# Kernel tuning notes

Measured on AMD Instinct MI355X. Metric: run time of the kernel, lower is better.

## Reference

```python
import jax, jax.numpy as jnp
import numpy as np

B, N, NT = 64, 1024, 100
DIM, KD, NH, D = 256, 16, 8, 64
DH = D * NH            # 512
NH_KD = KD * NH        # 128
H_KV = DH + NH_KD      # 640
PROJ_IN = DH + 1000    # 1512
NUM_OFFSETS = 10000    # 100x100 grid of (|dx|,|dy|)
EPS = 1e-5


def _bn_params(key, n):
    k1, k2, k3, k4 = jax.random.split(key, 4)
    gamma = 1.0 + 0.1 * jax.random.normal(k1, (n,), jnp.float32)
    beta = 0.1 * jax.random.normal(k2, (n,), jnp.float32)
    mean = 0.1 * jax.random.normal(k3, (n,), jnp.float32)
    var = 0.5 + jax.random.uniform(k4, (n,), jnp.float32)
    return gamma, beta, mean, var


def setup_inputs() -> dict:
    key = jax.random.key(0)
    ks = jax.random.split(key, 9)
    x = jax.random.normal(ks[0], (B, N, DIM), jnp.float32)
    text = jax.random.normal(ks[1], (NT, DIM), jnp.float32)
    kv_w = jax.random.normal(ks[2], (H_KV, DIM), jnp.float32) * (DIM ** -0.5)
    q_w = jax.random.normal(ks[3], (NH_KD, DIM), jnp.float32) * (DIM ** -0.5)
    proj_w = jax.random.normal(ks[4], (DIM, PROJ_IN), jnp.float32) * (PROJ_IN ** -0.5)
    kv_g, kv_b, kv_m, kv_v = _bn_params(ks[5], H_KV)
    q_g, q_b, q_m, q_v = _bn_params(ks[6], NH_KD)
    proj_g, proj_b, proj_m, proj_v = _bn_params(ks[7], DIM)
    biases = 0.02 * jax.random.normal(ks[8], (NH, NUM_OFFSETS), jnp.float32)
    return {
        'x': x, 'text': text,
        'kv_w': kv_w, 'kv_g': kv_g, 'kv_b': kv_b, 'kv_m': kv_m, 'kv_v': kv_v,
        'q_w': q_w, 'q_g': q_g, 'q_b': q_b, 'q_m': q_m, 'q_v': q_v,
        'proj_w': proj_w, 'proj_g': proj_g, 'proj_b': proj_b, 'proj_m': proj_m, 'proj_v': proj_v,
        'biases': biases, 'H': 32, 'W': 32,
    }


def _linear_bn(x, w, g, b, m, v):
    # Linear (no bias) followed by BatchNorm1d in eval mode, per feature.
    y = x @ w.T
    return (y - m) * (g * jax.lax.rsqrt(v + EPS)) + b


def _hardswish(x):
    return x * jnp.clip(x + 3.0, 0.0, 6.0) * (1.0 / 6.0)


def _bias_idx(nt, h, w):
    # text tokens laid on (row, col) grid of width 100; image tokens on HxW grid.
    t = jnp.arange(nt)
    p1x, p1y = t // 100, t % 100
    n = jnp.arange(h * w)
    p2x, p2y = n // w, n % w
    # offset id = |dx| * 100 + |dy| (first-appearance order of the offset dict)
    return jnp.abs(p1x[:, None] - p2x[None, :]) * 100 + jnp.abs(p1y[:, None] - p2y[None, :])


def reference(x, text, kv_w, kv_g, kv_b, kv_m, kv_v,
              q_w, q_g, q_b, q_m, q_v,
              proj_w, proj_g, proj_b, proj_m, proj_v,
              biases, H, W):
    b, n, _ = x.shape
    nt = text.shape[0]
    scale = KD ** -0.5

    kv = _linear_bn(x, kv_w, kv_g, kv_b, kv_m, kv_v).reshape(b, n, NH, KD + D)
    k = kv[..., :KD]                 # [B, N, NH, KD]
    v = kv[..., KD:]                 # [B, N, NH, D]
    q = _linear_bn(text, q_w, q_g, q_b, q_m, q_v).reshape(nt, NH, KD)  # [NT, NH, KD]

    idx = _bias_idx(nt, H, W)        # [NT, N] int32
    attn = jnp.einsum('thd,bnhd->bhtn', q, k) * scale + biases[:, idx]  # [B, NH, NT, N]
    attn = jax.nn.softmax(attn, axis=-1)

    v_flat = v.reshape(b, n, DH)                                    # [B, N, DH]
    attn_feat = attn.reshape(b, NH * nt, n).transpose(0, 2, 1)      # [B, N, NH*NT]
    comp = jnp.zeros((b, n, 1000 - nt * NH), x.dtype)
    v_cat = jnp.concatenate([v_flat, attn_feat, comp], axis=-1)     # [B, N, DH+1000]

    return _linear_bn(_hardswish(v_cat), proj_w, proj_g, proj_b, proj_m, proj_v)
```

## Files before the change

### kernel.cpp

```cpp
#include <hip/hip_runtime.h>
#include <hip/hip_bf16.h>

#define B_    64
#define N_    1024
#define NT_   100
#define DIM_  256
#define KD_   16
#define NH_   8
#define D_    64
#define DH_   512
#define HKV_  640
#define PROJIN_ 1512
#define KCAT_ 1312
#define EPS_  1e-5f
#define M_    (B_*N_)

typedef __attribute__((ext_vector_type(8))) short bf16x8;
typedef __attribute__((ext_vector_type(4))) float f32x4;

__device__ __forceinline__ int iabs(int x){ return x<0?-x:x; }
__device__ __forceinline__ unsigned short bfr(float f){ __hip_bfloat16 h=__float2bfloat16(f); return *(unsigned short*)&h; }
__device__ __forceinline__ float bfl(unsigned short u){ union{unsigned int i;float f;}c; c.i=(unsigned int)u<<16; return c.f; }

#define GLDS16(src, dst) __builtin_amdgcn_global_load_lds( \
    (const __attribute__((address_space(1))) void*)(src),  \
    (__attribute__((address_space(3))) void*)(dst), 16, 0, 0)

__global__ __launch_bounds__(256) void p0_cvt(
    const float* __restrict__ kvw, const float* __restrict__ pw,
    unsigned short* __restrict__ kvwb, unsigned short* __restrict__ pwb)
{
    const size_t stride = (size_t)gridDim.x * 256;
    const size_t i0 = (size_t)blockIdx.x * 256 + threadIdx.x;
    for (size_t q = i0; q < (size_t)HKV_*DIM_/4; q += stride) {
        float4 v = ((const float4*)kvw)[q];
        ushort4 o; o.x=bfr(v.x); o.y=bfr(v.y); o.z=bfr(v.z); o.w=bfr(v.w);
        ((ushort4*)kvwb)[q] = o;
    }
    for (size_t q = i0; q < (size_t)DIM_*KCAT_/4; q += stride) {
        const int row = (int)(q / (KCAT_/4)), cq = (int)(q % (KCAT_/4));
        float4 v = ((const float4*)(pw + (size_t)row*PROJIN_))[cq];
        ushort4 o; o.x=bfr(v.x); o.y=bfr(v.y); o.z=bfr(v.z); o.w=bfr(v.w);
        ((ushort4*)pwb)[q] = o;
    }
}

__global__ __launch_bounds__(256,2) void k1g(
    const float* __restrict__ x, const unsigned short* __restrict__ wb,
    const float* __restrict__ g, const float* __restrict__ bb,
    const float* __restrict__ mn, const float* __restrict__ vr,
    unsigned short* __restrict__ kb, unsigned short* __restrict__ vb)
{
    __shared__ unsigned short As[128*32];
    __shared__ unsigned short Bs[128*32];
    __shared__ unsigned short Ls[64*128];
    const int tid = threadIdx.x;
    const int wave = tid >> 6, lane = tid & 63;
    const int logical = (blockIdx.x & 7) * 320 + (blockIdx.x >> 3);
    const int nblk = logical % 5, mblk = logical / 5;
    const int m0 = mblk * 128, n0 = nblk * 128;
    const int wm = (wave >> 1) * 64, wn = (wave & 1) * 64;
    const int srow = lane >> 2, scol = (lane & 3) * 8;
    const int sr = tid >> 1, sh = (tid & 1) * 16;
    f32x4 acc[4][4];
    #pragma unroll
    for (int i=0;i<4;i++)
        #pragma unroll
        for (int j=0;j<4;j++) acc[i][j] = (f32x4){0.f,0.f,0.f,0.f};

    for (int k0 = 0; k0 < DIM_; k0 += 32) {
        #pragma unroll
        for (int i = 0; i < 2; i++) {
            const int rr = (wave*2 + i)*16 + srow;
            GLDS16(wb + (size_t)(n0+rr)*DIM_ + k0 + scol, Bs + (wave*2+i)*512);
        }
        {
            const float* xs = x + (size_t)(m0+sr)*DIM_ + k0 + sh;
            float4 v0 = ((const float4*)xs)[0], v1 = ((const float4*)xs)[1];
            float4 v2 = ((const float4*)xs)[2], v3 = ((const float4*)xs)[3];
            ushort4 a0, a1, b0, b1;
            a0.x=bfr(v0.x); a0.y=bfr(v0.y); a0.z=bfr(v0.z); a0.w=bfr(v0.w);
            a1.x=bfr(v1.x); a1.y=bfr(v1.y); a1.z=bfr(v1.z); a1.w=bfr(v1.w);
            b0.x=bfr(v2.x); b0.y=bfr(v2.y); b0.z=bfr(v2.z); b0.w=bfr(v2.w);
            b1.x=bfr(v3.x); b1.y=bfr(v3.y); b1.z=bfr(v3.z); b1.w=bfr(v3.w);
            *(ushort4*)&As[sr*32 + sh]      = a0;
            *(ushort4*)&As[sr*32 + sh + 4]  = a1;
            *(ushort4*)&As[sr*32 + sh + 8]  = b0;
            *(ushort4*)&As[sr*32 + sh + 12] = b1;
        }
        __syncthreads();
        bf16x8 af[4], bfv[4];
        #pragma unroll
        for (int f = 0; f < 4; f++) {
            af[f]  = *(const bf16x8*)&As[(wm + f*16 + (lane&15))*32 + (lane>>4)*8];
            bfv[f] = *(const bf16x8*)&Bs[(wn + f*16 + (lane&15))*32 + (lane>>4)*8];
        }
        #pragma unroll
        for (int fi = 0; fi < 4; fi++)
            #pragma unroll
            for (int fj = 0; fj < 4; fj++)
                acc[fi][fj] = __builtin_amdgcn_mfma_f32_16x16x32_bf16(af[fi], bfv[fj], acc[fi][fj], 0,0,0);
        __syncthreads();
    }

    #pragma unroll
    for (int pass = 0; pass < 2; ++pass) {
        if ((wave >> 1) == pass) {
            #pragma unroll
            for (int fj = 0; fj < 4; fj++) {
                const int col = wn + fj*16 + (lane & 15);
                const int gcol = n0 + col;
                const float s = g[gcol] * rsqrtf(vr[gcol] + EPS_);
                const float o = bb[gcol] - mn[gcol] * s;
                const bool vcol = (gcol - (gcol/80)*80) >= 16;
                #pragma unroll
                for (int fi = 0; fi < 4; fi++)
                    #pragma unroll
                    for (int r = 0; r < 4; r++) {
                        float v = acc[fi][fj][r] * s + o;
                        if (vcol) v = v * fminf(fmaxf(v + 3.f, 0.f), 6.f) * (1.f/6.f);
                        Ls[(fi*16 + (lane>>4)*4 + r)*128 + col] = bfr(v);
                    }
            }
        }
        __syncthreads();
        #pragma unroll
        for (int it = 0; it < 4; ++it) {
            const int row = it*16 + (tid >> 4);
            const int c8  = tid & 15;
            bf16x8 val = *(const bf16x8*)&Ls[row*128 + c8*8];
            const int gcol = n0 + c8*8;
            const int h = gcol / 80, rem = gcol - h*80;
            const int m = m0 + pass*64 + row;
            unsigned short* dst = (rem < 16)
                ? (kb + (size_t)m*128 + h*16 + rem)
                : (vb + (size_t)m*512 + h*64 + (rem - 16));
            *(bf16x8*)dst = val;
        }
        __syncthreads();
    }
}

__global__ __launch_bounds__(128) void k2_q(
    const float* __restrict__ text, const float* __restrict__ q_w,
    const float* __restrict__ g, const float* __restrict__ bb,
    const float* __restrict__ mn, const float* __restrict__ vr,
    float* __restrict__ q_out)
{
    __shared__ float ts[DIM_];
    const int t = blockIdx.x, j = threadIdx.x;
    for (int i = threadIdx.x; i < DIM_; i += 128) ts[i] = text[t * DIM_ + i];
    __syncthreads();
    float acc = 0.f;
    for (int k = 0; k < DIM_; k++) acc += ts[k] * q_w[j * DIM_ + k];
    const float s = g[j] * rsqrtf(vr[j] + EPS_);
    q_out[t * 128 + j] = acc * s + (bb[j] - mn[j] * s);
}

__global__ __launch_bounds__(256) void k3a(
    const unsigned short* __restrict__ kb, const float* __restrict__ qb,
    const float* __restrict__ biases, const int* __restrict__ Wp,
    float* __restrict__ wsinv)
{
    __shared__ unsigned short Kl[N_*16];
    __shared__ unsigned short Ql[112*32];
    __shared__ unsigned short bsl[3200];
    const int bh = blockIdx.x, b = bh >> 3, h = bh & 7;
    const int tid = threadIdx.x;
    const int wave = tid >> 6, lane = tid & 63;
    const int w = *Wp;

    #pragma unroll
    for (int i = 0; i < 8; i++) {
        const int C = i*256 + tid;
        const int n = C >> 1, half = C & 1;
        GLDS16(kb + (size_t)(b*N_ + n)*128 + h*16 + half*8, Kl + (i*256 + wave*64)*8);
    }
    for (int i = tid; i < 112*32; i += 256) {
        const int t = i >> 5, d = i & 31;
        Ql[i] = (t < NT_ && d < 16) ? bfr(qb[t*128 + h*16 + d]) : (unsigned short)0;
    }
    for (int i = tid; i < 3200; i += 256) bsl[i] = bfr(biases[h*10000 + i]);
    __syncthreads();

    const int kg = lane >> 4;
    for (int tt = wave; tt < 7; tt += 4) {
        bf16x8 qf = *(const bf16x8*)&Ql[(tt*16 + (lane&15))*32 + kg*8];
        float rs[4] = {0.f,0.f,0.f,0.f};
        const int tb = tt*16 + ((lane>>4)<<2);
        for (int nt = 0; nt < 64; nt++) {
            const int n = nt*16 + (lane & 15);
            bf16x8 kf = *(const bf16x8*)&Kl[n*16 + (kg&1)*8];
            f32x4 a = __builtin_amdgcn_mfma_f32_16x16x32_bf16(qf, kf, (f32x4){0.f,0.f,0.f,0.f}, 0,0,0);
            const int px = n / w;
            const int py = n - px*w;
            const int pxm = px*100;
            #pragma unroll
            for (int r = 0; r < 4; r++) {
                int dy = iabs(tb + r - py); dy = dy > 99 ? 99 : dy;
                rs[r] += __expf(fmaf(a[r], 0.25f, bfl(bsl[pxm + dy])));
            }
        }
        #pragma unroll
        for (int r = 0; r < 4; r++) {
            #pragma unroll
            for (int msk = 1; msk < 16; msk <<= 1) rs[r] += __shfl_xor(rs[r], msk);
        }
        if ((lane & 15) == 0) {
            #pragma unroll
            for (int r = 0; r < 4; r++)
                wsinv[(size_t)bh*112 + tb + r] = 1.0f / rs[r];
        }
    }
}

__global__ __launch_bounds__(256) void k3b(
    const unsigned short* __restrict__ kb, const float* __restrict__ qb,
    const float* __restrict__ biases, const int* __restrict__ Wp,
    const float* __restrict__ wsinv, unsigned short* __restrict__ attn_t)
{
    __shared__ unsigned short Kl[128*128];
    __shared__ unsigned short Ql[112*128];
    __shared__ unsigned short bsl[4000];
    __shared__ float invs[800];
    __shared__ unsigned short zbuf[8];
    const int bx = blockIdx.x, b = bx >> 3, n0 = (bx & 7) * 128;
    const int tid = threadIdx.x;
    const int wave = tid >> 6, lane = tid & 63;
    const int w = *Wp;
    const int pxlo = n0 / w;

    if (tid < 8) zbuf[tid] = 0;
    #pragma unroll
    for (int i = 0; i < 8; i++) {
        const int C = i*256 + tid;
        const int n = C >> 4, gslot = C & 15;
        const int h2g = gslot ^ (n & 7);
        GLDS16(kb + (size_t)(b*N_ + n0 + n)*128 + h2g*8, Kl + (i*256 + wave*64)*8);
    }
    for (int G = tid; G < 1792; G += 256) {
        const int t = G >> 4, dg = G & 15;
        ushort4 o0 = {0,0,0,0}, o1 = {0,0,0,0};
        if (t < NT_) {
            const float* src = qb + t*128 + dg*8;
            float4 v0 = *(const float4*)src, v1 = *(const float4*)(src+4);
            o0.x=bfr(v0.x); o0.y=bfr(v0.y); o0.z=bfr(v0.z); o0.w=bfr(v0.w);
            o1.x=bfr(v1.x); o1.y=bfr(v1.y); o1.z=bfr(v1.z); o1.w=bfr(v1.w);
        }
        unsigned short* dst = &Ql[t*128 + (dg ^ (t & 7))*8];
        *(ushort4*)dst = o0; *(ushort4*)(dst+4) = o1;
    }
    for (int i = tid; i < 4000; i += 256) {
        const int pr = i / 800, rem = i - pr*800;
        const int h = rem / 100, dy = rem - h*100;
        int row = pxlo + pr; row = row > 99 ? 99 : row;
        bsl[i] = bfr(biases[h*10000 + row*100 + dy]);
    }
    for (int i = tid; i < 800; i += 256) {
        const int h = i / 100, t = i - h*100;
        invs[i] = wsinv[(size_t)(b*8 + h)*112 + t];
    }
    __syncthreads();

    const int kg = lane >> 4;
    const int l15 = lane & 15, l7 = lane & 7;
    #pragma unroll
    for (int nn2 = 0; nn2 < 2; nn2++) {
        const int nn = wave + nn2*4;
        const int ng = n0 + nn*16 + l15;
        const int px = ng / w;
        const int prx = px - pxlo, py = ng - px*w;
        const size_t obase = (size_t)(b*N_ + ng)*800;
        const int nloc = nn*16 + l15;
        for (int h = 0; h < 8; h++) {
            const int h2 = h*2;
            bf16x8 kf = *(const bf16x8*)&Kl[nloc*128 + ((h2 | (kg&1)) ^ l7)*8];
            for (int tt = 0; tt < 7; tt++) {
                const int trow = tt*16 + l15;
                const unsigned short* aptr = (kg < 2)
                    ? &Ql[trow*128 + (((h2 | kg) ^ l7))*8] : zbuf;
                bf16x8 qf = *(const bf16x8*)aptr;
                f32x4 a = __builtin_amdgcn_mfma_f32_16x16x32_bf16(qf, kf, (f32x4){0.f,0.f,0.f,0.f}, 0,0,0);
                const int tb0 = tt*16 + (kg << 2);
                if (tb0 < NT_) {
                    ushort4 pk;
                    unsigned short* pkp = (unsigned short*)&pk;
                    #pragma unroll
                    for (int r = 0; r < 4; r++) {
                        const int t = tb0 + r;
                        int dy = iabs(t - py); dy = dy > 99 ? 99 : dy;
                        const float bbv = bfl(bsl[(prx*8 + h)*100 + dy]);
                        const float e = __expf(fmaf(a[r], 0.25f, bbv));
                        const float p = e * invs[h*100 + t];
                        pkp[r] = bfr(p * (p + 3.f) * (1.f/6.f));
                    }
                    *(ushort4*)(attn_t + obase + h*100 + tb0) = pk;
                }
            }
        }
    }
}

__global__ __launch_bounds__(512,2) void k4g(
    const unsigned short* __restrict__ vb, const unsigned short* __restrict__ attn_t,
    const unsigned short* __restrict__ pwb,
    const float* __restrict__ g, const float* __restrict__ bb,
    const float* __restrict__ mn, const float* __restrict__ vr,
    float* __restrict__ out)
{
    __shared__ unsigned short As[128*32];
    __shared__ unsigned short Bs[256*32];
    const int tid = threadIdx.x;
    const int wave = tid >> 6, lane = tid & 63;
    const int m0 = blockIdx.x * 128;
    const int wm = (wave >> 2) * 64, wn = (wave & 3) * 64;
    const int arow = tid >> 2, ac8 = (tid & 3) * 8;
    f32x4 acc[4][4];
    #pragma unroll
    for (int i=0;i<4;i++)
        #pragma unroll
        for (int j=0;j<4;j++) acc[i][j] = (f32x4){0.f,0.f,0.f,0.f};

    for (int ks = 0; ks < KCAT_/32; ks++) {
        const int k0 = ks * 32;
        {
            const size_t mrow = (size_t)(m0 + arow);
            const unsigned short* src = (k0 < DH_)
                ? (vb + mrow*512 + k0 + ac8)
                : (attn_t + mrow*800 + (k0 - DH_) + ac8);
            GLDS16(src, As + wave*512);
        }
        #pragma unroll
        for (int i = 0; i < 2; i++) {
            const int C = i*512 + tid;
            const int row = C >> 2, c8 = (C & 3)*8;
            GLDS16(pwb + (size_t)row*KCAT_ + k0 + c8, Bs + (i*512 + wave*64)*8);
        }
        __syncthreads();
        bf16x8 af[4], bfv[4];
        #pragma unroll
        for (int f = 0; f < 4; f++) {
            af[f]  = *(const bf16x8*)&As[(wm + f*16 + (lane&15))*32 + (lane>>4)*8];
            bfv[f] = *(const bf16x8*)&Bs[(wn + f*16 + (lane&15))*32 + (lane>>4)*8];
        }
        #pragma unroll
        for (int fi = 0; fi < 4; fi++)
            #pragma unroll
            for (int fj = 0; fj < 4; fj++)
                acc[fi][fj] = __builtin_amdgcn_mfma_f32_16x16x32_bf16(af[fi], bfv[fj], acc[fi][fj], 0,0,0);
        __syncthreads();
    }
    #pragma unroll
    for (int fj = 0; fj < 4; fj++) {
        const int col = wn + fj*16 + (lane & 15);
        const float s = g[col] * rsqrtf(vr[col] + EPS_);
        const float o = bb[col] - mn[col] * s;
        #pragma unroll
        for (int fi = 0; fi < 4; fi++)
            #pragma unroll
            for (int r = 0; r < 4; r++) {
                const int m = m0 + wm + fi*16 + (lane>>4)*4 + r;
                out[(size_t)m * DIM_ + col] = acc[fi][fj][r] * s + o;
            }
    }
}

extern "C" void kernel_launch(void* const* d_in, const int* in_sizes, int n_in,
                              void* d_out, int out_size, void* d_ws, size_t ws_size,
                              hipStream_t stream) {
    const float* x      = (const float*)d_in[0];
    const float* text   = (const float*)d_in[1];
    const float* kv_w   = (const float*)d_in[2];
    const float* kv_g   = (const float*)d_in[3];
    const float* kv_b   = (const float*)d_in[4];
    const float* kv_m   = (const float*)d_in[5];
    const float* kv_v   = (const float*)d_in[6];
    const float* q_w    = (const float*)d_in[7];
    const float* q_g    = (const float*)d_in[8];
    const float* q_b    = (const float*)d_in[9];
    const float* q_m    = (const float*)d_in[10];
    const float* q_v    = (const float*)d_in[11];
    const float* proj_w = (const float*)d_in[12];
    const float* proj_g = (const float*)d_in[13];
    const float* proj_b = (const float*)d_in[14];
    const float* proj_m = (const float*)d_in[15];
    const float* proj_v = (const float*)d_in[16];
    const float* biases = (const float*)d_in[17];
    const int*   Wp     = (const int*)d_in[19];
    float* out = (float*)d_out;

    char* w = (char*)d_ws;
    size_t off = 0;
    auto alloc = [&](size_t bytes) { void* p = w + off; off += (bytes + 255) & ~255ull; return p; };
    unsigned short* kvwb  = (unsigned short*)alloc((size_t)HKV_*DIM_*2);
    unsigned short* pwb   = (unsigned short*)alloc((size_t)DIM_*KCAT_*2);
    unsigned short* kbuf  = (unsigned short*)alloc((size_t)M_*128*2);
    unsigned short* vbuf  = (unsigned short*)alloc((size_t)M_*512*2);
    unsigned short* attnt = (unsigned short*)alloc((size_t)M_*800*2);
    float*          qbuf  = (float*)alloc((size_t)NT_*128*4);
    float*          wsinv = (float*)alloc((size_t)B_*NH_*112*4);

    p0_cvt<<<256, 256, 0, stream>>>(kv_w, proj_w, kvwb, pwb);
    k1g<<<2560, 256, 0, stream>>>(x, kvwb, kv_g, kv_b, kv_m, kv_v, kbuf, vbuf);
    k2_q<<<NT_, 128, 0, stream>>>(text, q_w, q_g, q_b, q_m, q_v, qbuf);
    k3a<<<B_*NH_, 256, 0, stream>>>(kbuf, qbuf, biases, Wp, wsinv);
    k3b<<<B_*NH_, 256, 0, stream>>>(kbuf, qbuf, biases, Wp, wsinv, attnt);
    k4g<<<M_/128, 512, 0, stream>>>(vbuf, attnt, pwb, proj_g, proj_b, proj_m, proj_v, out);
}
```

Baseline: 371.8 us.

## Fuse softmax passes, defer normalization into projection GEMM, swizzle and double-buffer LDS

The separate k3b pass that recomputed QK scores is removed. The row-sum pass (k3f) now also writes the unnormalized exponentials to attn_t in bf16, and the projection GEMM applies the inverse row sums plus hardswish when it stages those tiles into LDS. The k1g and k4g GEMMs gain XOR-swizzled LDS layouts, register prefetch or double-buffered tiles, and k1g's occupancy hint is raised with its shared buffers aliased. This trades a full extra attention recompute for bf16 rounding of the unnormalized exponentials and a more complex synchronized pipeline.

Result: faster. 349.8 us (-5.9%).

```diff
diff --git a/kernel.cpp b/kernel.cpp
--- a/kernel.cpp
+++ b/kernel.cpp
@@ -21,6 +21,7 @@
 __device__ __forceinline__ int iabs(int x){ return x<0?-x:x; }
 __device__ __forceinline__ unsigned short bfr(float f){ __hip_bfloat16 h=__float2bfloat16(f); return *(unsigned short*)&h; }
 __device__ __forceinline__ float bfl(unsigned short u){ union{unsigned int i;float f;}c; c.i=(unsigned int)u<<16; return c.f; }
+__device__ __forceinline__ int swzofs(int row, int slot){ return (row*4 + (slot ^ ((row>>1)&3)))*8; }
 
 #define GLDS16(src, dst) __builtin_amdgcn_global_load_lds( \
     (const __attribute__((address_space(1))) void*)(src),  \
@@ -45,64 +46,85 @@
     }
 }
 
-__global__ __launch_bounds__(256,2) void k1g(
+__global__ __launch_bounds__(256,4) void k1g(
     const float* __restrict__ x, const unsigned short* __restrict__ wb,
     const float* __restrict__ g, const float* __restrict__ bb,
     const float* __restrict__ mn, const float* __restrict__ vr,
     unsigned short* __restrict__ kb, unsigned short* __restrict__ vb)
 {
-    __shared__ unsigned short As[128*32];
-    __shared__ unsigned short Bs[128*32];
-    __shared__ unsigned short Ls[64*128];
+    __shared__ unsigned short sbuf[8192];
+    unsigned short* As = sbuf;
+    unsigned short* Bs = sbuf + 4096;
     const int tid = threadIdx.x;
     const int wave = tid >> 6, lane = tid & 63;
     const int logical = (blockIdx.x & 7) * 320 + (blockIdx.x >> 3);
     const int nblk = logical % 5, mblk = logical / 5;
     const int m0 = mblk * 128, n0 = nblk * 128;
     const int wm = (wave >> 1) * 64, wn = (wave & 1) * 64;
-    const int srow = lane >> 2, scol = (lane & 3) * 8;
-    const int sr = tid >> 1, sh = (tid & 1) * 16;
+    const int arow = tid >> 2, aslot = tid & 3;
     f32x4 acc[4][4];
     #pragma unroll
     for (int i=0;i<4;i++)
         #pragma unroll
         for (int j=0;j<4;j++) acc[i][j] = (f32x4){0.f,0.f,0.f,0.f};
 
-    for (int k0 = 0; k0 < DIM_; k0 += 32) {
+    float4 xv[2][2][2];
+    #pragma unroll
+    for (int c = 0; c < 2; c++) {
+        const float4* p = (const float4*)(x + (size_t)(m0 + arow + c*64)*DIM_ + aslot*8);
+        xv[0][c][0] = p[0]; xv[0][c][1] = p[1];
+    }
+
+    #pragma unroll
+    for (int ks = 0; ks < 8; ks++) {
+        const int k0 = ks*32;
+        if (ks) __builtin_amdgcn_s_barrier();
         #pragma unroll
         for (int i = 0; i < 2; i++) {
-            const int rr = (wave*2 + i)*16 + srow;
-            GLDS16(wb + (size_t)(n0+rr)*DIM_ + k0 + scol, Bs + (wave*2+i)*512);
-        }
-        {
-            const float* xs = x + (size_t)(m0+sr)*DIM_ + k0 + sh;
-            float4 v0 = ((const float4*)xs)[0], v1 = ((const float4*)xs)[1];
-            float4 v2 = ((const float4*)xs)[2], v3 = ((const float4*)xs)[3];
-            ushort4 a0, a1, b0, b1;
-            a0.x=bfr(v0.x); a0.y=bfr(v0.y); a0.z=bfr(v0.z); a0.w=bfr(v0.w);
-            a1.x=bfr(v1.x); a1.y=bfr(v1.y); a1.z=bfr(v1.z); a1.w=bfr(v1.w);
-            b0.x=bfr(v2.x); b0.y=bfr(v2.y); b0.z=bfr(v2.z); b0.w=bfr(v2.w);
-            b1.x=bfr(v3.x); b1.y=bfr(v3.y); b1.z=bfr(v3.z); b1.w=bfr(v3.w);
-            *(ushort4*)&As[sr*32 + sh]      = a0;
-            *(ushort4*)&As[sr*32 + sh + 4]  = a1;
-            *(ushort4*)&As[sr*32 + sh + 8]  = b0;
-            *(ushort4*)&As[sr*32 + sh + 12] = b1;
-        }
-        __syncthreads();
+            const int C = i*256 + tid;
+            const int row = C>>2, slot = C&3;
+            GLDS16(wb + (size_t)(n0+row)*DIM_ + k0 + ((slot ^ ((row>>1)&3))<<3),
+                   Bs + (i*256 + wave*64)*8);
+        }
+        __builtin_amdgcn_sched_barrier(0);
+        if (ks < 7) {
+            #pragma unroll
+            for (int c = 0; c < 2; c++) {
+                const float4* p = (const float4*)(x + (size_t)(m0 + arow + c*64)*DIM_ + k0 + 32 + aslot*8);
+                xv[(ks+1)&1][c][0] = p[0]; xv[(ks+1)&1][c][1] = p[1];
+            }
+        }
+        __builtin_amdgcn_sched_barrier(0);
+        #pragma unroll
+        for (int c = 0; c < 2; c++) {
+            const int row = arow + c*64;
+            float4 v0 = xv[ks&1][c][0], v1 = xv[ks&1][c][1];
+            ushort4 lo, hi;
+            lo.x=bfr(v0.x); lo.y=bfr(v0.y); lo.z=bfr(v0.z); lo.w=bfr(v0.w);
+            hi.x=bfr(v1.x); hi.y=bfr(v1.y); hi.z=bfr(v1.z); hi.w=bfr(v1.w);
+            unsigned short* d = &As[swzofs(row, aslot)];
+            *(ushort4*)d = lo; *(ushort4*)(d+4) = hi;
+        }
+        if (ks < 7) asm volatile("s_waitcnt vmcnt(2) lgkmcnt(0)" ::: "memory");
+        else        asm volatile("s_waitcnt vmcnt(0) lgkmcnt(0)" ::: "memory");
+        __builtin_amdgcn_sched_barrier(0);
+        __builtin_amdgcn_s_barrier();
+
         bf16x8 af[4], bfv[4];
         #pragma unroll
         for (int f = 0; f < 4; f++) {
-            af[f]  = *(const bf16x8*)&As[(wm + f*16 + (lane&15))*32 + (lane>>4)*8];
-            bfv[f] = *(const bf16x8*)&Bs[(wn + f*16 + (lane&15))*32 + (lane>>4)*8];
+            af[f]  = *(const bf16x8*)&As[swzofs(wm + f*16 + (lane&15), lane>>4)];
+            bfv[f] = *(const bf16x8*)&Bs[swzofs(wn + f*16 + (lane&15), lane>>4)];
         }
         #pragma unroll
         for (int fi = 0; fi < 4; fi++)
             #pragma unroll
             for (int fj = 0; fj < 4; fj++)
                 acc[fi][fj] = __builtin_amdgcn_mfma_f32_16x16x32_bf16(af[fi], bfv[fj], acc[fi][fj], 0,0,0);
-        __syncthreads();
-    }
-
+    }
+    __syncthreads();
+
+    unsigned short* Ls = sbuf;
     #pragma unroll
     for (int pass = 0; pass < 2; ++pass) {
         if ((wave >> 1) == pass) {
@@ -157,10 +179,10 @@
     q_out[t * 128 + j] = acc * s + (bb[j] - mn[j] * s);
 }
 
-__global__ __launch_bounds__(256) void k3a(
+__global__ __launch_bounds__(256) void k3f(
     const unsigned short* __restrict__ kb, const float* __restrict__ qb,
     const float* __restrict__ biases, const int* __restrict__ Wp,
-    float* __restrict__ wsinv)
+    float* __restrict__ wsinv, unsigned short* __restrict__ attn_t)
 {
     __shared__ unsigned short Kl[N_*16];
     __shared__ unsigned short Ql[112*32];
@@ -187,7 +209,8 @@
     for (int tt = wave; tt < 7; tt += 4) {
         bf16x8 qf = *(const bf16x8*)&Ql[(tt*16 + (lane&15))*32 + kg*8];
         float rs[4] = {0.f,0.f,0.f,0.f};
-        const int tb = tt*16 + ((lane>>4)<<2);
+        const int tb = tt*16 + (kg<<2);
+        const bool doStore = tb < NT_;
         for (int nt = 0; nt < 64; nt++) {
             const int n = nt*16 + (lane & 15);
             bf16x8 kf = *(const bf16x8*)&Kl[n*16 + (kg&1)*8];
@@ -195,11 +218,17 @@
             const int px = n / w;
             const int py = n - px*w;
             const int pxm = px*100;
+            ushort4 pk;
+            unsigned short* pkp = (unsigned short*)&pk;
             #pragma unroll
             for (int r = 0; r < 4; r++) {
                 int dy = iabs(tb + r - py); dy = dy > 99 ? 99 : dy;
-                rs[r] += __expf(fmaf(a[r], 0.25f, bfl(bsl[pxm + dy])));
-            }
+                const float e = __expf(fmaf(a[r], 0.25f, bfl(bsl[pxm + dy])));
+                rs[r] += e;
+                pkp[r] = bfr(e);
+            }
+            if (doStore)
+                *(ushort4*)(attn_t + (size_t)(b*N_ + n)*800 + h*100 + tb) = pk;
         }
         #pragma unroll
         for (int r = 0; r < 4; r++) {
@@ -214,142 +243,97 @@
     }
 }
 
-__global__ __launch_bounds__(256) void k3b(
-    const unsigned short* __restrict__ kb, const float* __restrict__ qb,
-    const float* __restrict__ biases, const int* __restrict__ Wp,
-    const float* __restrict__ wsinv, unsigned short* __restrict__ attn_t)
-{
-    __shared__ unsigned short Kl[128*128];
-    __shared__ unsigned short Ql[112*128];
-    __shared__ unsigned short bsl[4000];
-    __shared__ float invs[800];
-    __shared__ unsigned short zbuf[8];
-    const int bx = blockIdx.x, b = bx >> 3, n0 = (bx & 7) * 128;
-    const int tid = threadIdx.x;
-    const int wave = tid >> 6, lane = tid & 63;
-    const int w = *Wp;
-    const int pxlo = n0 / w;
-
-    if (tid < 8) zbuf[tid] = 0;
-    #pragma unroll
-    for (int i = 0; i < 8; i++) {
-        const int C = i*256 + tid;
-        const int n = C >> 4, gslot = C & 15;
-        const int h2g = gslot ^ (n & 7);
-        GLDS16(kb + (size_t)(b*N_ + n0 + n)*128 + h2g*8, Kl + (i*256 + wave*64)*8);
-    }
-    for (int G = tid; G < 1792; G += 256) {
-        const int t = G >> 4, dg = G & 15;
-        ushort4 o0 = {0,0,0,0}, o1 = {0,0,0,0};
-        if (t < NT_) {
-            const float* src = qb + t*128 + dg*8;
-            float4 v0 = *(const float4*)src, v1 = *(const float4*)(src+4);
-            o0.x=bfr(v0.x); o0.y=bfr(v0.y); o0.z=bfr(v0.z); o0.w=bfr(v0.w);
-            o1.x=bfr(v1.x); o1.y=bfr(v1.y); o1.z=bfr(v1.z); o1.w=bfr(v1.w);
-        }
-        unsigned short* dst = &Ql[t*128 + (dg ^ (t & 7))*8];
-        *(ushort4*)dst = o0; *(ushort4*)(dst+4) = o1;
-    }
-    for (int i = tid; i < 4000; i += 256) {
-        const int pr = i / 800, rem = i - pr*800;
-        const int h = rem / 100, dy = rem - h*100;
-        int row = pxlo + pr; row = row > 99 ? 99 : row;
-        bsl[i] = bfr(biases[h*10000 + row*100 + dy]);
-    }
-    for (int i = tid; i < 800; i += 256) {
-        const int h = i / 100, t = i - h*100;
-        invs[i] = wsinv[(size_t)(b*8 + h)*112 + t];
-    }
-    __syncthreads();
-
-    const int kg = lane >> 4;
-    const int l15 = lane & 15, l7 = lane & 7;
-    #pragma unroll
-    for (int nn2 = 0; nn2 < 2; nn2++) {
-        const int nn = wave + nn2*4;
-        const int ng = n0 + nn*16 + l15;
-        const int px = ng / w;
-        const int prx = px - pxlo, py = ng - px*w;
-        const size_t obase = (size_t)(b*N_ + ng)*800;
-        const int nloc = nn*16 + l15;
-        for (int h = 0; h < 8; h++) {
-            const int h2 = h*2;
-            bf16x8 kf = *(const bf16x8*)&Kl[nloc*128 + ((h2 | (kg&1)) ^ l7)*8];
-            for (int tt = 0; tt < 7; tt++) {
-                const int trow = tt*16 + l15;
-                const unsigned short* aptr = (kg < 2)
-                    ? &Ql[trow*128 + (((h2 | kg) ^ l7))*8] : zbuf;
-                bf16x8 qf = *(const bf16x8*)aptr;
-                f32x4 a = __builtin_amdgcn_mfma_f32_16x16x32_bf16(qf, kf, (f32x4){0.f,0.f,0.f,0.f}, 0,0,0);
-                const int tb0 = tt*16 + (kg << 2);
-                if (tb0 < NT_) {
-                    ushort4 pk;
-                    unsigned short* pkp = (unsigned short*)&pk;
-                    #pragma unroll
-                    for (int r = 0; r < 4; r++) {
-                        const int t = tb0 + r;
-                        int dy = iabs(t - py); dy = dy > 99 ? 99 : dy;
-                        const float bbv = bfl(bsl[(prx*8 + h)*100 + dy]);
-                        const float e = __expf(fmaf(a[r], 0.25f, bbv));
-                        const float p = e * invs[h*100 + t];
-                        pkp[r] = bfr(p * (p + 3.f) * (1.f/6.f));
-                    }
-                    *(ushort4*)(attn_t + obase + h*100 + tb0) = pk;
-                }
-            }
-        }
-    }
-}
-
 __global__ __launch_bounds__(512,2) void k4g(
-    const unsigned short* __restrict__ vb, const unsigned short* __restrict__ attn_t,
-    const unsigned short* __restrict__ pwb,
+    const unsigned short* __restrict__ vb, const unsigned short* __restrict__ et,
+    const unsigned short* __restrict__ pwb, const float* __restrict__ wsinvf,
     const float* __restrict__ g, const float* __restrict__ bb,
     const float* __restrict__ mn, const float* __restrict__ vr,
     float* __restrict__ out)
 {
-    __shared__ unsigned short As[128*32];
-    __shared__ unsigned short Bs[256*32];
+    __shared__ unsigned short AS[2][4096];
+    __shared__ unsigned short BS[2][8192];
+    __shared__ float invf[800];
     const int tid = threadIdx.x;
     const int wave = tid >> 6, lane = tid & 63;
     const int m0 = blockIdx.x * 128;
+    const int b  = blockIdx.x >> 3;
     const int wm = (wave >> 2) * 64, wn = (wave & 3) * 64;
-    const int arow = tid >> 2, ac8 = (tid & 3) * 8;
+    const int arow = tid >> 2, aslot = tid & 3;
     f32x4 acc[4][4];
     #pragma unroll
     for (int i=0;i<4;i++)
         #pragma unroll
         for (int j=0;j<4;j++) acc[i][j] = (f32x4){0.f,0.f,0.f,0.f};
 
-    for (int ks = 0; ks < KCAT_/32; ks++) {
-        const int k0 = ks * 32;
-        {
-            const size_t mrow = (size_t)(m0 + arow);
-            const unsigned short* src = (k0 < DH_)
-                ? (vb + mrow*512 + k0 + ac8)
-                : (attn_t + mrow*800 + (k0 - DH_) + ac8);
-            GLDS16(src, As + wave*512);
-        }
+    for (int i = tid; i < 800; i += 512) {
+        const int h = i / 100;
+        invf[i] = wsinvf[(size_t)(b*8 + h)*112 + (i - h*100)];
+    }
+    {
+        GLDS16(vb + (size_t)(m0+arow)*512 + ((aslot ^ ((arow>>1)&3))<<3), AS[0] + wave*512);
         #pragma unroll
         for (int i = 0; i < 2; i++) {
             const int C = i*512 + tid;
-            const int row = C >> 2, c8 = (C & 3)*8;
-            GLDS16(pwb + (size_t)row*KCAT_ + k0 + c8, Bs + (i*512 + wave*64)*8);
-        }
-        __syncthreads();
+            const int row = C>>2, slot = C&3;
+            GLDS16(pwb + (size_t)row*KCAT_ + ((slot ^ ((row>>1)&3))<<3), BS[0] + (i*512 + wave*64)*8);
+        }
+    }
+    asm volatile("s_waitcnt vmcnt(0)" ::: "memory");
+    __builtin_amdgcn_s_barrier();
+
+    for (int ks = 0; ks < 41; ks++) {
+        const int cur = ks & 1, nxt = cur ^ 1;
+        const bool hasNext = (ks < 40);
+        uint4 ev;
+        bool nextAttn = false;
+        if (hasNext) {
+            const int k0n = (ks+1)*32;
+            if (k0n >= DH_) {
+                nextAttn = true;
+                ev = *(const uint4*)(et + (size_t)(m0+arow)*800 + (k0n - DH_) + aslot*8);
+            } else {
+                GLDS16(vb + (size_t)(m0+arow)*512 + k0n + ((aslot ^ ((arow>>1)&3))<<3),
+                       AS[nxt] + wave*512);
+            }
+            #pragma unroll
+            for (int i = 0; i < 2; i++) {
+                const int C = i*512 + tid;
+                const int row = C>>2, slot = C&3;
+                GLDS16(pwb + (size_t)row*KCAT_ + k0n + ((slot ^ ((row>>1)&3))<<3),
+                       BS[nxt] + (i*512 + wave*64)*8);
+            }
+        }
         bf16x8 af[4], bfv[4];
         #pragma unroll
         for (int f = 0; f < 4; f++) {
-            af[f]  = *(const bf16x8*)&As[(wm + f*16 + (lane&15))*32 + (lane>>4)*8];
-            bfv[f] = *(const bf16x8*)&Bs[(wn + f*16 + (lane&15))*32 + (lane>>4)*8];
+            af[f]  = *(const bf16x8*)&AS[cur][swzofs(wm + f*16 + (lane&15), lane>>4)];
+            bfv[f] = *(const bf16x8*)&BS[cur][swzofs(wn + f*16 + (lane&15), lane>>4)];
         }
         #pragma unroll
         for (int fi = 0; fi < 4; fi++)
             #pragma unroll
             for (int fj = 0; fj < 4; fj++)
                 acc[fi][fj] = __builtin_amdgcn_mfma_f32_16x16x32_bf16(af[fi], bfv[fj], acc[fi][fj], 0,0,0);
-        __syncthreads();
-    }
+        if (nextAttn) {
+            const int cb = (ks+1)*32 - DH_ + aslot*8;
+            float4 iv0 = *(const float4*)&invf[cb];
+            float4 iv1 = *(const float4*)&invf[cb+4];
+            const float iv[8] = {iv0.x,iv0.y,iv0.z,iv0.w,iv1.x,iv1.y,iv1.z,iv1.w};
+            const unsigned short* u16 = (const unsigned short*)&ev;
+            unsigned short o[8];
+            #pragma unroll
+            for (int j = 0; j < 8; j++) {
+                const float p = bfl(u16[j]) * iv[j];
+                o[j] = bfr(p * (p + 3.f) * (1.f/6.f));
+            }
+            unsigned short* d = &AS[nxt][swzofs(arow, aslot)];
+            *(ushort4*)d = *(ushort4*)&o[0];
+            *(ushort4*)(d+4) = *(ushort4*)&o[4];
+        }
+        asm volatile("s_waitcnt vmcnt(0) lgkmcnt(0)" ::: "memory");
+        __builtin_amdgcn_s_barrier();
+    }
+
     #pragma unroll
     for (int fj = 0; fj < 4; fj++) {
         const int col = wn + fj*16 + (lane & 15);
@@ -403,7 +387,6 @@
     p0_cvt<<<256, 256, 0, stream>>>(kv_w, proj_w, kvwb, pwb);
     k1g<<<2560, 256, 0, stream>>>(x, kvwb, kv_g, kv_b, kv_m, kv_v, kbuf, vbuf);
     k2_q<<<NT_, 128, 0, stream>>>(text, q_w, q_g, q_b, q_m, q_v, qbuf);
-    k3a<<<B_*NH_, 256, 0, stream>>>(kbuf, qbuf, biases, Wp, wsinv);
-    k3b<<<B_*NH_, 256, 0, stream>>>(kbuf, qbuf, biases, Wp, wsinv, attnt);
-    k4g<<<M_/128, 512, 0, stream>>>(vbuf, attnt, pwb, proj_g, proj_b, proj_m, proj_v, out);
-}
+    k3f<<<B_*NH_, 256, 0, stream>>>(kbuf, qbuf, biases, Wp, wsinv, attnt);
+    k4g<<<M_/128, 512, 0, stream>>>(vbuf, attnt, pwb, wsinv, proj_g, proj_b, proj_m, proj_v, out);
+}
```
